# Kernel optimization log

Hardware: AMD Instinct MI355X
Metric: run time of the kernel (lower is better)

## Reference

```python
import jax, jax.numpy as jnp
import numpy as np

DIM = 384
WIN = 7
HEADS = 12
N = WIN * WIN
B_ = 4096
NW = 64


def _relative_position_index(ws: int) -> np.ndarray:
    coords = np.stack(np.meshgrid(np.arange(ws), np.arange(ws), indexing='ij'))  # (2, ws, ws)
    flat = coords.reshape(2, -1)  # (2, N)
    rel = flat[:, :, None] - flat[:, None, :]  # (2, N, N)
    rel = rel.transpose(1, 2, 0).copy()  # (N, N, 2)
    rel[:, :, 0] += ws - 1
    rel[:, :, 1] += ws - 1
    rel[:, :, 0] *= 2 * ws - 1
    return rel.sum(-1).astype(np.int32)  # (N, N)


def setup_inputs() -> dict:
    key = jax.random.key(0)
    ks = jax.random.split(key, 6)
    x = jax.random.normal(ks[0], (B_, N, DIM), dtype=jnp.float32)
    mask = jnp.zeros((NW, N, N), dtype=jnp.float32)
    bias_table = 0.02 * jax.random.normal(ks[1], ((2 * WIN - 1) ** 2, HEADS), dtype=jnp.float32)
    qkv_w = jax.random.normal(ks[2], (3 * DIM, DIM), dtype=jnp.float32) / np.sqrt(DIM)
    qkv_b = jnp.zeros((3 * DIM,), dtype=jnp.float32)
    proj_w = jax.random.normal(ks[3], (DIM, DIM), dtype=jnp.float32) / np.sqrt(DIM)
    proj_b = jnp.zeros((DIM,), dtype=jnp.float32)
    rel_index = jnp.asarray(_relative_position_index(WIN))  # (N, N) int32
    return {"x": x, "mask": mask, "bias_table": bias_table, "qkv_w": qkv_w,
            "qkv_b": qkv_b, "proj_w": proj_w, "proj_b": proj_b, "rel_index": rel_index}


def reference(x, mask, bias_table, qkv_w, qkv_b, proj_w, proj_b, rel_index):
    Bw, n, c = x.shape
    h = bias_table.shape[1]
    d = c // h
    scale = d ** (-0.5)
    # qkv projection: (Bw, n, 3, h, d)
    qkv = (x @ qkv_w.T + qkv_b).reshape(Bw, n, 3, h, d)
    qkv = jnp.transpose(qkv, (2, 0, 3, 1, 4))  # (3, Bw, h, n, d)
    q, k, v = qkv[0], qkv[1], qkv[2]
    attn = jnp.einsum('bhqd,bhkd->bhqk', q * scale, k)  # (Bw, h, n, n)
    bias = bias_table[rel_index]  # (n, n, h)
    attn = attn + jnp.transpose(bias, (2, 0, 1))[None]  # broadcast over Bw
    nW = mask.shape[0]
    attn = attn.reshape(Bw // nW, nW, h, n, n) + mask[None, :, None]
    attn = attn.reshape(Bw, h, n, n)
    attn = jax.nn.softmax(attn, axis=-1)
    out = jnp.einsum('bhqk,bhkd->bhqd', attn, v)  # (Bw, h, n, d)
    out = jnp.transpose(out, (0, 2, 1, 3)).reshape(Bw, n, c)
    return out @ proj_w.T + proj_b
```

## Files before the change

kernel.cpp:

```cpp
#include <hip/hip_runtime.h>
#include <hip/hip_bf16.h>

#define DIM   384
#define NWIN  49
#define HEADS 12
#define SCALE 0.17677669529663687f

typedef unsigned short ushort;
using bf16x8 = __attribute__((ext_vector_type(8))) short;
using u16x4  = __attribute__((ext_vector_type(4))) ushort;
using f32x4  = __attribute__((ext_vector_type(4))) float;

__device__ __forceinline__ ushort f2bf(float f) {
  unsigned u = __float_as_uint(f);
  u += 0x7fff + ((u >> 16) & 1);
  return (ushort)(u >> 16);
}

typedef __attribute__((address_space(1))) const void gas_void;
typedef __attribute__((address_space(3))) void las_void;

__device__ __forceinline__ void gload16(const ushort* g, ushort* l) {
  __builtin_amdgcn_global_load_lds((gas_void*)g, (las_void*)l, 16, 0, 0);
}

__global__ void prep_kernel(const float* __restrict__ qkv_w, const float* __restrict__ proj_w,
                            const float* __restrict__ bias_table, const int* __restrict__ rel_index,
                            const float* __restrict__ mask, const float* __restrict__ qkv_b,
                            ushort* __restrict__ wqb, ushort* __restrict__ wpb,
                            float* __restrict__ qbF, float* __restrict__ bmF) {
  int i0 = blockIdx.x * 256 + threadIdx.x;
  int stride = gridDim.x * 256;
  for (int i = i0; i < 1152 * 384; i += stride) {
    float v = qkv_w[i];
    if (i < 384 * 384) v *= SCALE;
    wqb[i] = f2bf(v);
  }
  for (int i = i0; i < 384 * 384; i += stride) wpb[i] = f2bf(proj_w[i]);
  for (int i = i0; i < 1152; i += stride) qbF[i] = qkv_b[i] * (i < 384 ? SCALE : 1.f);
  for (int i = i0; i < 64 * HEADS * 4 * 4 * 64 * 4; i += stride) {
    int r = i & 3, lane = (i >> 2) & 63, kt = (i >> 8) & 3, wq = (i >> 10) & 3;
    int hw = i >> 12;
    int h = hw % HEADS, wdx = hw / HEADS;
    int q = wq * 16 + (lane >> 4) * 4 + r;
    int key = kt * 16 + (lane & 15);
    float v;
    if (q < NWIN)
      v = (key < NWIN) ? bias_table[rel_index[q * NWIN + key] * HEADS + h]
                         + mask[wdx * (NWIN * NWIN) + q * NWIN + key]
                       : -3.0e38f;
    else
      v = 0.f;
    bmF[i] = v;
  }
}

__global__ __launch_bounds__(256, 2) void qkv_attn_kernel(
    const float* __restrict__ x, const float* __restrict__ qbF,
    const ushort* __restrict__ wqb, const float* __restrict__ bmF,
    ushort* __restrict__ aog)
{
  __shared__ ushort wb[2 * 12288];
  __shared__ ushort qs[64 * 36];
  __shared__ ushort ks[64 * 36];
  __shared__ ushort vt[32 * 74];

  const int blk = blockIdx.x;
  const int tid = threadIdx.x;
  const int w = tid >> 6, l = tid & 63;
  const int c = l & 15, g = l >> 4;
  const int wm = w >> 1, wn = w & 1;
  const int wq = w;
  const int wdx = blk & 63;
  const float LOG2E = 1.4426950408889634f;

  auto stage_qkv = [&](int h, int kc, int buf) {
    #pragma unroll
    for (int s = 0; s < 6; ++s) {
      int i = s * 256 + tid;
      int n = i >> 4, g16 = i & 15;
      int grow = (n >> 5) * 384 + h * 32 + (n & 31);
      int sg = (g16 & 8) | ((g16 & 7) ^ (n & 7));
      gload16(wqb + (size_t)grow * DIM + kc * 128 + (sg << 3),
              wb + buf * 12288 + i * 8);
    }
  };

  bf16x8 areg[2][12] = {};
  auto compute_qkv = [&](int kcC, int buf, f32x4 (&acc)[2][3]) {
    const ushort* wcb = wb + buf * 12288;
    #pragma unroll
    for (int kk = 0; kk < 4; ++kk) {
      int sB = ((kk * 4 + g) ^ (c & 7)) << 3;
      #pragma unroll
      for (int nt = 0; nt < 3; ++nt) {
        int n = (wn * 3 + nt) * 16 + c;
        bf16x8 bb = *(const bf16x8*)&wcb[n * 128 + sB];
        acc[0][nt] = __builtin_amdgcn_mfma_f32_16x16x32_bf16(areg[0][kcC * 4 + kk], bb, acc[0][nt], 0, 0, 0);
        acc[1][nt] = __builtin_amdgcn_mfma_f32_16x16x32_bf16(areg[1][kcC * 4 + kk], bb, acc[1][nt], 0, 0, 0);
      }
    }
  };

  {
    const float* xb = x + (size_t)blk * (NWIN * DIM);
    for (int i = tid; i < 4704; i += 256) {
      float4 f = ((const float4*)xb)[i];
      int row = i / 96, c4 = i - row * 96;
      u16x4 v4 = { f2bf(f.x), f2bf(f.y), f2bf(f.z), f2bf(f.w) };
      *(u16x4*)&wb[row * 384 + c4 * 4] = v4;
    }
  }
  __syncthreads();
  #pragma unroll
  for (int mt = 0; mt < 2; ++mt) {
    int row = wm * 32 + mt * 16 + c;
    if (row < NWIN) {
      #pragma unroll
      for (int kg = 0; kg < 12; ++kg)
        areg[mt][kg] = *(const bf16x8*)&wb[row * 384 + kg * 32 + g * 8];
    }
  }
  __syncthreads();
  stage_qkv(0, 0, 0);
  stage_qkv(0, 1, 1);
  __syncthreads();

  for (int h = 0; h < HEADS; ++h) {
    f32x4 acc[2][3] = {};
    const int par = h & 1;

    compute_qkv(0, par, acc);
    __syncthreads();
    stage_qkv(h, 2, par);

    compute_qkv(1, par ^ 1, acc);
    __syncthreads();
    if (h < 11) stage_qkv(h + 1, 0, par ^ 1);

    compute_qkv(2, par, acc);
    __syncthreads();
    if (h < 11) stage_qkv(h + 1, 1, par);

    #pragma unroll
    for (int nt = 0; nt < 3; ++nt) {
      int gnt = wn * 3 + nt;
      int which = gnt >> 1;
      int d = (gnt & 1) * 16 + c;
      float qb_ = qbF[which * 384 + h * 32 + d];
      #pragma unroll
      for (int mt = 0; mt < 2; ++mt) {
        #pragma unroll
        for (int r = 0; r < 4; ++r) {
          int tok = wm * 32 + mt * 16 + g * 4 + r;
          float v = acc[mt][nt][r] + qb_;
          if (which == 0)      qs[tok * 36 + d] = f2bf(v);
          else if (which == 1) ks[tok * 36 + d] = f2bf(v);
          else                 vt[d * 74 + tok] = f2bf(v);
        }
      }
    }
    __syncthreads();

    const f32x4* bw4 = (const f32x4*)(bmF + ((((size_t)(wdx * HEADS + h)) * 4 + wq) * 4 * 64 + l) * 4);
    f32x4 bmv[4];
    #pragma unroll
    for (int kt = 0; kt < 4; ++kt) bmv[kt] = bw4[kt * 64];

    f32x4 sacc[4] = {};
    {
      bf16x8 aq = *(const bf16x8*)&qs[(wq * 16 + c) * 36 + g * 8];
      #pragma unroll
      for (int kt = 0; kt < 4; ++kt) {
        bf16x8 bk = *(const bf16x8*)&ks[(kt * 16 + c) * 36 + g * 8];
        sacc[kt] = __builtin_amdgcn_mfma_f32_16x16x32_bf16(aq, bk, sacc[kt], 0, 0, 0);
      }
    }
    float p[4][4];
    #pragma unroll
    for (int r = 0; r < 4; ++r) {
      float s0 = sacc[0][r] + bmv[0][r], s1 = sacc[1][r] + bmv[1][r];
      float s2 = sacc[2][r] + bmv[2][r], s3 = sacc[3][r] + bmv[3][r];
      float mx = fmaxf(fmaxf(s0, s1), fmaxf(s2, s3));
      mx = fmaxf(mx, __shfl_xor(mx, 1, 64));
      mx = fmaxf(mx, __shfl_xor(mx, 2, 64));
      mx = fmaxf(mx, __shfl_xor(mx, 4, 64));
      mx = fmaxf(mx, __shfl_xor(mx, 8, 64));
      float p0 = __builtin_exp2f((s0 - mx) * LOG2E);
      float p1 = __builtin_exp2f((s1 - mx) * LOG2E);
      float p2 = __builtin_exp2f((s2 - mx) * LOG2E);
      float p3 = __builtin_exp2f((s3 - mx) * LOG2E);
      float sum = p0 + p1 + p2 + p3;
      sum += __shfl_xor(sum, 1, 64);
      sum += __shfl_xor(sum, 2, 64);
      sum += __shfl_xor(sum, 4, 64);
      sum += __shfl_xor(sum, 8, 64);
      float inv = 1.0f / sum;
      p[0][r] = p0 * inv; p[1][r] = p1 * inv; p[2][r] = p2 * inv; p[3][r] = p3 * inv;
    }
    f32x4 pacc[2] = {};
    #pragma unroll
    for (int kkh = 0; kkh < 2; ++kkh) {
      #pragma unroll
      for (int t = 0; t < 2; ++t) {
        int kt = kkh * 2 + t;
        #pragma unroll
        for (int r = 0; r < 4; ++r)
          qs[(wq * 16 + g * 4 + r) * 36 + t * 16 + c] = f2bf(p[kt][r]);
      }
      bf16x8 ap = *(const bf16x8*)&qs[(wq * 16 + c) * 36 + g * 8];
      #pragma unroll
      for (int dt = 0; dt < 2; ++dt) {
        bf16x8 bv = *(const bf16x8*)&vt[(dt * 16 + c) * 74 + kkh * 32 + g * 8];
        pacc[dt] = __builtin_amdgcn_mfma_f32_16x16x32_bf16(ap, bv, pacc[dt], 0, 0, 0);
      }
    }
    #pragma unroll
    for (int dt = 0; dt < 2; ++dt) {
      #pragma unroll
      for (int rr = 0; rr < 4; ++rr) {
        int tok = wq * 16 + g * 4 + rr;
        if (tok < NWIN)
          aog[((size_t)blk * NWIN + tok) * DIM + h * 32 + dt * 16 + c] = f2bf(pacc[dt][rr]);
      }
    }
    __syncthreads();
  }
}

__global__ __launch_bounds__(256, 2) void proj_kernel(
    const ushort* __restrict__ ao, const ushort* __restrict__ wpb,
    const float* __restrict__ proj_b, float* __restrict__ out)
{
  extern __shared__ ushort sm3[];
  ushort* lA = sm3;
  ushort* lB = sm3 + 16384;

  const int blk = blockIdx.x;
  const int bM = blk / 3, bN = blk - bM * 3;
  const int m0 = bM * 128, n0 = bN * 128;
  const int tid = threadIdx.x;
  const int w = tid >> 6, l = tid & 63;
  const int c = l & 15, g = l >> 4;
  const int wm = w >> 1, wn = w & 1;

  auto stageA = [&](int kc, int buf) {
    #pragma unroll
    for (int s = 0; s < 4; ++s) {
      int i = s * 256 + tid;
      int row = i >> 3, g16 = i & 7;
      gload16(ao + (size_t)(m0 + row) * DIM + kc * 64 + ((g16 ^ (row & 7)) << 3),
              lA + buf * 8192 + i * 8);
    }
  };
  auto stageB = [&](int kc, int buf) {
    #pragma unroll
    for (int s = 0; s < 4; ++s) {
      int i = s * 256 + tid;
      int row = i >> 3, g16 = i & 7;
      gload16(wpb + (size_t)(n0 + row) * DIM + kc * 64 + ((g16 ^ (row & 7)) << 3),
              lB + buf * 8192 + i * 8);
    }
  };

  f32x4 acc[4][4] = {};
  stageA(0, 0); stageB(0, 0);
  stageA(1, 1); stageB(1, 1);
  __syncthreads();

  for (int kc = 0; kc < 6; ++kc) {
    const ushort* A = lA + (kc & 1) * 8192;
    const ushort* B = lB + (kc & 1) * 8192;
    #pragma unroll
    for (int kk = 0; kk < 2; ++kk) {
      int swz = ((kk * 4 + g) ^ (c & 7)) << 3;
      bf16x8 af[4], bfr[4];
      #pragma unroll
      for (int mt = 0; mt < 4; ++mt)
        af[mt] = *(const bf16x8*)&A[(wm * 64 + mt * 16 + c) * 64 + swz];
      #pragma unroll
      for (int nt = 0; nt < 4; ++nt)
        bfr[nt] = *(const bf16x8*)&B[(wn * 64 + nt * 16 + c) * 64 + swz];
      #pragma unroll
      for (int mt = 0; mt < 4; ++mt)
        #pragma unroll
        for (int nt = 0; nt < 4; ++nt)
          acc[mt][nt] = __builtin_amdgcn_mfma_f32_16x16x32_bf16(af[mt], bfr[nt], acc[mt][nt], 0, 0, 0);
    }
    __syncthreads();
    if (kc + 2 < 6) { stageA(kc + 2, kc & 1); stageB(kc + 2, kc & 1); }
  }

  #pragma unroll
  for (int nt = 0; nt < 4; ++nt) {
    int col = n0 + wn * 64 + nt * 16 + c;
    float pb = proj_b[col];
    #pragma unroll
    for (int mt = 0; mt < 4; ++mt) {
      #pragma unroll
      for (int r = 0; r < 4; ++r) {
        int row = m0 + wm * 64 + mt * 16 + g * 4 + r;
        out[(size_t)row * DIM + col] = acc[mt][nt][r] + pb;
      }
    }
  }
}

#define WB_OFF 0
#define QS_OFF 24576
#define KS_OFF 29696
#define VT_OFF 34816
#define AO_OFF 39424
#define SMEM_US 77056

__global__ __launch_bounds__(512, 2) void winattn_fused(
    const float* __restrict__ x, const float* __restrict__ qbF,
    const float* __restrict__ proj_b, const ushort* __restrict__ wqb,
    const ushort* __restrict__ wpb, const float* __restrict__ bmF,
    float* __restrict__ out)
{
  extern __shared__ ushort smem[];
  ushort* wb = smem + WB_OFF;
  ushort* ao = smem + AO_OFF;

  const int blk = blockIdx.x;
  const int tid = threadIdx.x;
  const int w = tid >> 6, l = tid & 63;
  const int c = l & 15, g = l >> 4;
  const int wm = w >> 1, wn = w & 1;
  const int win = w >> 2, wq = w & 3;
  const float LOG2E = 1.4426950408889634f;

  ushort* qsw = smem + QS_OFF + win * 2560;
  ushort* ksw = smem + KS_OFF + win * 2560;
  ushort* vtw = smem + VT_OFF + win * 2304;
  ushort* psw = qsw;

  auto stage_qkv = [&](int h, int kc, int buf) {
    #pragma unroll
    for (int s = 0; s < 3; ++s) {
      int i = s * 512 + tid;
      int n = i >> 4, g16 = i & 15;
      int grow = (n >> 5) * 384 + h * 32 + (n & 31);
      int sg = (g16 & 8) | ((g16 & 7) ^ (n & 7));
      gload16(wqb + (size_t)grow * DIM + kc * 128 + (sg << 3), wb + buf * 12288 + i * 8);
    }
  };
  auto stage_proj = [&](int nb, int kc, int buf) {
    #pragma unroll
    for (int s = 0; s < 3; ++s) {
      int i = s * 512 + tid;
      int n = i >> 4, g16 = i & 15;
      int grow = nb * 96 + n;
      int sg = (g16 & 8) | ((g16 & 7) ^ (n & 7));
      gload16(wpb + (size_t)grow * DIM + kc * 128 + (sg << 3), wb + buf * 12288 + i * 8);
    }
  };

  bf16x8 areg[2][12] = {};
  auto compute_qkv = [&](int kcC, int buf, f32x4 (&acc)[2][3]) {
    const ushort* wcb = wb + buf * 12288;
    #pragma unroll
    for (int kk = 0; kk < 4; ++kk) {
      int sB = ((kk * 4 + g) ^ (c & 7)) << 3;
      #pragma unroll
      for (int nt = 0; nt < 3; ++nt) {
        int n = (wn * 3 + nt) * 16 + c;
        bf16x8 bb = *(const bf16x8*)&wcb[n * 128 + sB];
        acc[0][nt] = __builtin_amdgcn_mfma_f32_16x16x32_bf16(areg[0][kcC * 4 + kk], bb, acc[0][nt], 0, 0, 0);
        acc[1][nt] = __builtin_amdgcn_mfma_f32_16x16x32_bf16(areg[1][kcC * 4 + kk], bb, acc[1][nt], 0, 0, 0);
      }
    }
  };
  auto compute_proj = [&](int kcC, int buf, f32x4 (&acc)[2][3]) {
    const ushort* wcb = wb + buf * 12288;
    int r0 = wm * 32 + c;      if (r0 >= 98) r0 -= 64;
    int r1 = wm * 32 + 16 + c; if (r1 >= 98) r1 -= 64;
    #pragma unroll
    for (int kk = 0; kk < 4; ++kk) {
      int p = kcC * 16 + kk * 4 + g;
      int sw = (p ^ (c & 7)) << 3;
      bf16x8 a0 = *(const bf16x8*)&ao[r0 * 384 + sw];
      bf16x8 a1 = *(const bf16x8*)&ao[r1 * 384 + sw];
      int sB = ((kk * 4 + g) ^ (c & 7)) << 3;
      #pragma unroll
      for (int nt = 0; nt < 3; ++nt) {
        int n = (wn * 3 + nt) * 16 + c;
        bf16x8 bb = *(const bf16x8*)&wcb[n * 128 + sB];
        acc[0][nt] = __builtin_amdgcn_mfma_f32_16x16x32_bf16(a0, bb, acc[0][nt], 0, 0, 0);
        acc[1][nt] = __builtin_amdgcn_mfma_f32_16x16x32_bf16(a1, bb, acc[1][nt], 0, 0, 0);
      }
    }
  };

  stage_qkv(0, 0, 0);
  stage_qkv(0, 1, 1);
  {
    const float* xb = x + (size_t)blk * (2 * NWIN * DIM);
    for (int i = tid; i < 9408; i += 512) {
      float4 f = ((const float4*)xb)[i];
      int row = i / 96, c4 = i - row * 96;
      int k = c4 * 4;
      int gr = k >> 3;
      u16x4 v4 = { f2bf(f.x), f2bf(f.y), f2bf(f.z), f2bf(f.w) };
      *(u16x4*)&ao[row * 384 + ((gr ^ (row & 7)) << 3) + (k & 7)] = v4;
    }
  }
  __syncthreads();
  #pragma unroll
  for (int mt = 0; mt < 2; ++mt) {
    int row = wm * 32 + mt * 16 + c;
    int wi = row >> 6, tok = row & 63;
    if (tok < NWIN) {
      int ar = wi * 49 + tok;
      #pragma unroll
      for (int kg = 0; kg < 12; ++kg)
        areg[mt][kg] = *(const bf16x8*)&ao[ar * 384 + (((kg * 4 + g) ^ (ar & 7)) << 3)];
    }
  }

  for (int h = 0; h < HEADS; ++h) {
    f32x4 acc[2][3] = {};
    const int par = h & 1;
    compute_qkv(0, par, acc);
    __syncthreads();
    stage_qkv(h, 2, par);
    compute_qkv(1, par ^ 1, acc);
    __syncthreads();
    if (h < 11) stage_qkv(h + 1, 0, par ^ 1); else stage_proj(0, 0, par ^ 1);
    compute_qkv(2, par, acc);
    __syncthreads();
    if (h < 11) stage_qkv(h + 1, 1, par); else stage_proj(0, 1, par);
    {
      int winE = wm >> 1;
      ushort* qsE = smem + QS_OFF + winE * 2560;
      ushort* ksE = smem + KS_OFF + winE * 2560;
      ushort* vtE = smem + VT_OFF + winE * 2304;
      #pragma unroll
      for (int nt = 0; nt < 3; ++nt) {
        int gnt = wn * 3 + nt;
        int which = gnt >> 1;
        int d = (gnt & 1) * 16 + c;
        float qb_ = qbF[which * 384 + h * 32 + d];
        #pragma unroll
        for (int mt = 0; mt < 2; ++mt) {
          #pragma unroll
          for (int r = 0; r < 4; ++r) {
            int tok = (wm & 1) * 32 + mt * 16 + g * 4 + r;
            float v = acc[mt][nt][r] + qb_;
            if (which == 0)      qsE[tok * 40 + d] = f2bf(v);
            else if (which == 1) ksE[tok * 40 + d] = f2bf(v);
            else                 vtE[d * 72 + tok] = f2bf(v);
          }
        }
      }
    }
    __syncthreads();

    const int wdx = ((blk << 1) + win) & 63;
    const f32x4* bw4 = (const f32x4*)(bmF + ((((size_t)(wdx * HEADS + h)) * 4 + wq) * 4 * 64 + l) * 4);
    f32x4 bmv[4];
    #pragma unroll
    for (int kt = 0; kt < 4; ++kt) bmv[kt] = bw4[kt * 64];

    f32x4 sacc[4] = {};
    {
      bf16x8 aq = *(const bf16x8*)&qsw[(wq * 16 + c) * 40 + g * 8];
      #pragma unroll
      for (int kt = 0; kt < 4; ++kt) {
        bf16x8 bk = *(const bf16x8*)&ksw[(kt * 16 + c) * 40 + g * 8];
        sacc[kt] = __builtin_amdgcn_mfma_f32_16x16x32_bf16(aq, bk, sacc[kt], 0, 0, 0);
      }
    }
    float p[4][4];
    #pragma unroll
    for (int r = 0; r < 4; ++r) {
      float s0 = sacc[0][r] + bmv[0][r], s1 = sacc[1][r] + bmv[1][r];
      float s2 = sacc[2][r] + bmv[2][r], s3 = sacc[3][r] + bmv[3][r];
      float mx = fmaxf(fmaxf(s0, s1), fmaxf(s2, s3));
      mx = fmaxf(mx, __shfl_xor(mx, 1, 64));
      mx = fmaxf(mx, __shfl_xor(mx, 2, 64));
      mx = fmaxf(mx, __shfl_xor(mx, 4, 64));
      mx = fmaxf(mx, __shfl_xor(mx, 8, 64));
      float p0 = __builtin_exp2f((s0 - mx) * LOG2E);
      float p1 = __builtin_exp2f((s1 - mx) * LOG2E);
      float p2 = __builtin_exp2f((s2 - mx) * LOG2E);
      float p3 = __builtin_exp2f((s3 - mx) * LOG2E);
      float sum = p0 + p1 + p2 + p3;
      sum += __shfl_xor(sum, 1, 64);
      sum += __shfl_xor(sum, 2, 64);
      sum += __shfl_xor(sum, 4, 64);
      sum += __shfl_xor(sum, 8, 64);
      float inv = 1.0f / sum;
      p[0][r] = p0 * inv; p[1][r] = p1 * inv; p[2][r] = p2 * inv; p[3][r] = p3 * inv;
    }
    f32x4 pacc2[2] = {};
    #pragma unroll
    for (int kkh = 0; kkh < 2; ++kkh) {
      #pragma unroll
      for (int t = 0; t < 2; ++t) {
        int kt = kkh * 2 + t;
        #pragma unroll
        for (int r = 0; r < 4; ++r)
          psw[(wq * 16 + g * 4 + r) * 40 + t * 16 + c] = f2bf(p[kt][r]);
      }
      bf16x8 ap = *(const bf16x8*)&psw[(wq * 16 + c) * 40 + g * 8];
      #pragma unroll
      for (int dt = 0; dt < 2; ++dt) {
        bf16x8 bv = *(const bf16x8*)&vtw[(dt * 16 + c) * 72 + kkh * 32 + g * 8];
        pacc2[dt] = __builtin_amdgcn_mfma_f32_16x16x32_bf16(ap, bv, pacc2[dt], 0, 0, 0);
      }
    }
    #pragma unroll
    for (int dt = 0; dt < 2; ++dt) {
      int gr0 = h * 4 + dt * 2 + (c >> 3);
      #pragma unroll
      for (int rr = 0; rr < 4; ++rr) {
        int tok = wq * 16 + g * 4 + rr;
        int row0 = win * 49 + tok;
        if (tok < NWIN)
          ao[row0 * 384 + (((gr0 ^ (row0 & 7)) << 3) | (c & 7))] = f2bf(pacc2[dt][rr]);
      }
    }
    __syncthreads();
  }

  __syncthreads();
  for (int nb = 0; nb < 4; ++nb) {
    f32x4 acc[2][3] = {};
    const int pb0 = (nb * 3) & 1;
    compute_proj(0, pb0, acc);
    __syncthreads();
    stage_proj(nb, 2, pb0);
    compute_proj(1, pb0 ^ 1, acc);
    __syncthreads();
    if (nb < 3) stage_proj(nb + 1, 0, pb0 ^ 1);
    compute_proj(2, pb0, acc);
    __syncthreads();
    if (nb < 3) stage_proj(nb + 1, 1, pb0);
    #pragma unroll
    for (int nt = 0; nt < 3; ++nt) {
      int col = nb * 96 + (wn * 3 + nt) * 16 + c;
      float pb = proj_b[col];
      #pragma unroll
      for (int mt = 0; mt < 2; ++mt) {
        #pragma unroll
        for (int r = 0; r < 4; ++r) {
          int mrow = wm * 32 + mt * 16 + g * 4 + r;
          if (mrow < 98) {
            int wi = mrow >= NWIN;
            int tok = mrow - (wi ? NWIN : 0);
            out[((size_t)((blk << 1) + wi) * NWIN + tok) * DIM + col] = acc[mt][nt][r] + pb;
          }
        }
      }
    }
  }
}

extern "C" void kernel_launch(void* const* d_in, const int* in_sizes, int n_in,
                              void* d_out, int out_size, void* d_ws, size_t ws_size,
                              hipStream_t stream) {
  const float* x          = (const float*)d_in[0];
  const float* mask       = (const float*)d_in[1];
  const float* bias_table = (const float*)d_in[2];
  const float* qkv_w      = (const float*)d_in[3];
  const float* qkv_b      = (const float*)d_in[4];
  const float* proj_w     = (const float*)d_in[5];
  const float* proj_b     = (const float*)d_in[6];
  const int*   rel_index  = (const int*)d_in[7];
  float* out = (float*)d_out;

  ushort* wqb = (ushort*)d_ws;
  ushort* wpb = (ushort*)((char*)d_ws + 884736);
  float*  qbF = (float*)((char*)d_ws + 1179648);
  float*  bmF = (float*)((char*)d_ws + 1184256);
  ushort* aog = (ushort*)((char*)d_ws + 13767168);
  const size_t NEED = 13767168ull + 154140672ull;

  prep_kernel<<<1024, 256, 0, stream>>>(qkv_w, proj_w, bias_table, rel_index, mask, qkv_b,
                                        wqb, wpb, qbF, bmF);

  if (ws_size >= NEED) {
    qkv_attn_kernel<<<4096, 256, 0, stream>>>(x, qbF, wqb, bmF, aog);
    hipFuncSetAttribute((const void*)proj_kernel,
                        hipFuncAttributeMaxDynamicSharedMemorySize, 65536);
    proj_kernel<<<4704, 256, 65536, stream>>>(aog, wpb, proj_b, out);
  } else {
    hipFuncSetAttribute((const void*)winattn_fused,
                        hipFuncAttributeMaxDynamicSharedMemorySize, SMEM_US * 2);
    winattn_fused<<<2048, 512, SMEM_US * 2, stream>>>(x, qbF, proj_b, wqb, wpb, bmF, out);
  }
}
```

Before: 798.6 us.

## Process two windows per block in qkv_attn kernel to share staged weights

The QKV+attention kernel now handles two windows per 512-thread block instead of one window per 256-thread block. Each head's weight slices, loaded into LDS, are reused by both windows, and the weight staging and barriers are amortized across both. Per-window q/k/v buffers use new padded strides in dynamic shared memory. The cost is a larger LDS footprint per block and bigger barriers across 8 waves, which may reduce occupancy.

After: 937.6 us. +17.4%, slower.

```diff
diff --git a/kernel.cpp b/kernel.cpp
--- a/kernel.cpp
+++ b/kernel.cpp
@@ -55,29 +55,32 @@
   }
 }
 
-__global__ __launch_bounds__(256, 2) void qkv_attn_kernel(
+#define WB_OFF 0
+#define QS_OFF 24576
+#define KS_OFF 29440
+#define VT_OFF 34304
+#define SMEM2_US 39040
+
+__global__ __launch_bounds__(512, 2) void qkv_attn_kernel(
     const float* __restrict__ x, const float* __restrict__ qbF,
     const ushort* __restrict__ wqb, const float* __restrict__ bmF,
     ushort* __restrict__ aog)
 {
-  __shared__ ushort wb[2 * 12288];
-  __shared__ ushort qs[64 * 36];
-  __shared__ ushort ks[64 * 36];
-  __shared__ ushort vt[32 * 74];
+  extern __shared__ ushort smem[];
+  ushort* wb = smem + WB_OFF;
 
   const int blk = blockIdx.x;
   const int tid = threadIdx.x;
   const int w = tid >> 6, l = tid & 63;
   const int c = l & 15, g = l >> 4;
   const int wm = w >> 1, wn = w & 1;
-  const int wq = w;
-  const int wdx = blk & 63;
+  const int win = w >> 2, wq = w & 3;
   const float LOG2E = 1.4426950408889634f;
 
   auto stage_qkv = [&](int h, int kc, int buf) {
     #pragma unroll
-    for (int s = 0; s < 6; ++s) {
-      int i = s * 256 + tid;
+    for (int s = 0; s < 3; ++s) {
+      int i = s * 512 + tid;
       int n = i >> 4, g16 = i & 15;
       int grow = (n >> 5) * 384 + h * 32 + (n & 31);
       int sg = (g16 & 8) | ((g16 & 7) ^ (n & 7));
@@ -102,26 +105,28 @@
     }
   };
 
-  {
-    const float* xb = x + (size_t)blk * (NWIN * DIM);
-    for (int i = tid; i < 4704; i += 256) {
+  #pragma unroll
+  for (int wi = 0; wi < 2; ++wi) {
+    const float* xb = x + (size_t)((blk << 1) + wi) * (NWIN * DIM);
+    for (int i = tid; i < 4704; i += 512) {
       float4 f = ((const float4*)xb)[i];
       int row = i / 96, c4 = i - row * 96;
       u16x4 v4 = { f2bf(f.x), f2bf(f.y), f2bf(f.z), f2bf(f.w) };
       *(u16x4*)&wb[row * 384 + c4 * 4] = v4;
     }
-  }
-  __syncthreads();
-  #pragma unroll
-  for (int mt = 0; mt < 2; ++mt) {
-    int row = wm * 32 + mt * 16 + c;
-    if (row < NWIN) {
-      #pragma unroll
-      for (int kg = 0; kg < 12; ++kg)
-        areg[mt][kg] = *(const bf16x8*)&wb[row * 384 + kg * 32 + g * 8];
-    }
-  }
-  __syncthreads();
+    __syncthreads();
+    #pragma unroll
+    for (int mt = 0; mt < 2; ++mt) {
+      int row = wm * 32 + mt * 16 + c;
+      int tok = row & 63;
+      if ((row >> 6) == wi && tok < NWIN) {
+        #pragma unroll
+        for (int kg = 0; kg < 12; ++kg)
+          areg[mt][kg] = *(const bf16x8*)&wb[tok * 384 + kg * 32 + g * 8];
+      }
+    }
+    __syncthreads();
+  }
   stage_qkv(0, 0, 0);
   stage_qkv(0, 1, 1);
   __syncthreads();
@@ -142,26 +147,36 @@
     __syncthreads();
     if (h < 11) stage_qkv(h + 1, 1, par);
 
-    #pragma unroll
-    for (int nt = 0; nt < 3; ++nt) {
-      int gnt = wn * 3 + nt;
-      int which = gnt >> 1;
-      int d = (gnt & 1) * 16 + c;
-      float qb_ = qbF[which * 384 + h * 32 + d];
-      #pragma unroll
-      for (int mt = 0; mt < 2; ++mt) {
+    {
+      int winE = wm >> 1;
+      ushort* qsE = smem + QS_OFF + winE * 2432;
+      ushort* ksE = smem + KS_OFF + winE * 2432;
+      ushort* vtE = smem + VT_OFF + winE * 2368;
+      #pragma unroll
+      for (int nt = 0; nt < 3; ++nt) {
+        int gnt = wn * 3 + nt;
+        int which = gnt >> 1;
+        int d = (gnt & 1) * 16 + c;
+        float qb_ = qbF[which * 384 + h * 32 + d];
         #pragma unroll
-        for (int r = 0; r < 4; ++r) {
-          int tok = wm * 32 + mt * 16 + g * 4 + r;
-          float v = acc[mt][nt][r] + qb_;
-          if (which == 0)      qs[tok * 36 + d] = f2bf(v);
-          else if (which == 1) ks[tok * 36 + d] = f2bf(v);
-          else                 vt[d * 74 + tok] = f2bf(v);
+        for (int mt = 0; mt < 2; ++mt) {
+          #pragma unroll
+          for (int r = 0; r < 4; ++r) {
+            int tok = (wm & 1) * 32 + mt * 16 + g * 4 + r;
+            float v = acc[mt][nt][r] + qb_;
+            if (which == 0)      qsE[tok * 38 + d] = f2bf(v);
+            else if (which == 1) ksE[tok * 38 + d] = f2bf(v);
+            else                 vtE[d * 74 + tok] = f2bf(v);
+          }
         }
       }
     }
     __syncthreads();
 
+    ushort* qsw = smem + QS_OFF + win * 2432;
+    ushort* ksw = smem + KS_OFF + win * 2432;
+    ushort* vtw = smem + VT_OFF + win * 2368;
+    const int wdx = ((blk << 1) + win) & 63;
     const f32x4* bw4 = (const f32x4*)(bmF + ((((size_t)(wdx * HEADS + h)) * 4 + wq) * 4 * 64 + l) * 4);
     f32x4 bmv[4];
     #pragma unroll
@@ -169,10 +184,10 @@
 
     f32x4 sacc[4] = {};
     {
-      bf16x8 aq = *(const bf16x8*)&qs[(wq * 16 + c) * 36 + g * 8];
+      bf16x8 aq = *(const bf16x8*)&qsw[(wq * 16 + c) * 38 + g * 8];
       #pragma unroll
       for (int kt = 0; kt < 4; ++kt) {
-        bf16x8 bk = *(const bf16x8*)&ks[(kt * 16 + c) * 36 + g * 8];
+        bf16x8 bk = *(const bf16x8*)&ksw[(kt * 16 + c) * 38 + g * 8];
         sacc[kt] = __builtin_amdgcn_mfma_f32_16x16x32_bf16(aq, bk, sacc[kt], 0, 0, 0);
       }
     }
@@ -206,12 +221,12 @@
         int kt = kkh * 2 + t;
         #pragma unroll
         for (int r = 0; r < 4; ++r)
-          qs[(wq * 16 + g * 4 + r) * 36 + t * 16 + c] = f2bf(p[kt][r]);
-      }
-      bf16x8 ap = *(const bf16x8*)&qs[(wq * 16 + c) * 36 + g * 8];
+          qsw[(wq * 16 + g * 4 + r) * 38 + t * 16 + c] = f2bf(p[kt][r]);
+      }
+      bf16x8 ap = *(const bf16x8*)&qsw[(wq * 16 + c) * 38 + g * 8];
       #pragma unroll
       for (int dt = 0; dt < 2; ++dt) {
-        bf16x8 bv = *(const bf16x8*)&vt[(dt * 16 + c) * 74 + kkh * 32 + g * 8];
+        bf16x8 bv = *(const bf16x8*)&vtw[(dt * 16 + c) * 74 + kkh * 32 + g * 8];
         pacc[dt] = __builtin_amdgcn_mfma_f32_16x16x32_bf16(ap, bv, pacc[dt], 0, 0, 0);
       }
     }
@@ -221,7 +236,8 @@
       for (int rr = 0; rr < 4; ++rr) {
         int tok = wq * 16 + g * 4 + rr;
         if (tok < NWIN)
-          aog[((size_t)blk * NWIN + tok) * DIM + h * 32 + dt * 16 + c] = f2bf(pacc[dt][rr]);
+          aog[((size_t)((blk << 1) + win) * NWIN + tok) * DIM + h * 32 + dt * 16 + c] =
+              f2bf(pacc[dt][rr]);
       }
     }
     __syncthreads();
@@ -306,12 +322,12 @@
   }
 }
 
-#define WB_OFF 0
-#define QS_OFF 24576
-#define KS_OFF 29696
-#define VT_OFF 34816
-#define AO_OFF 39424
-#define SMEM_US 77056
+#define FWB_OFF 0
+#define FQS_OFF 24576
+#define FKS_OFF 29696
+#define FVT_OFF 34816
+#define FAO_OFF 39424
+#define FSMEM_US 77056
 
 __global__ __launch_bounds__(512, 2) void winattn_fused(
     const float* __restrict__ x, const float* __restrict__ qbF,
@@ -320,8 +336,8 @@
     float* __restrict__ out)
 {
   extern __shared__ ushort smem[];
-  ushort* wb = smem + WB_OFF;
-  ushort* ao = smem + AO_OFF;
+  ushort* wb = smem + FWB_OFF;
+  ushort* ao = smem + FAO_OFF;
 
   const int blk = blockIdx.x;
   const int tid = threadIdx.x;
@@ -331,9 +347,9 @@
   const int win = w >> 2, wq = w & 3;
   const float LOG2E = 1.4426950408889634f;
 
-  ushort* qsw = smem + QS_OFF + win * 2560;
-  ushort* ksw = smem + KS_OFF + win * 2560;
-  ushort* vtw = smem + VT_OFF + win * 2304;
+  ushort* qsw = smem + FQS_OFF + win * 2560;
+  ushort* ksw = smem + FKS_OFF + win * 2560;
+  ushort* vtw = smem + FVT_OFF + win * 2304;
   ushort* psw = qsw;
 
   auto stage_qkv = [&](int h, int kc, int buf) {
@@ -433,9 +449,9 @@
     if (h < 11) stage_qkv(h + 1, 1, par); else stage_proj(0, 1, par);
     {
       int winE = wm >> 1;
-      ushort* qsE = smem + QS_OFF + winE * 2560;
-      ushort* ksE = smem + KS_OFF + winE * 2560;
-      ushort* vtE = smem + VT_OFF + winE * 2304;
+      ushort* qsE = smem + FQS_OFF + winE * 2560;
+      ushort* ksE = smem + FKS_OFF + winE * 2560;
+      ushort* vtE = smem + FVT_OFF + winE * 2304;
       #pragma unroll
       for (int nt = 0; nt < 3; ++nt) {
         int gnt = wn * 3 + nt;
@@ -582,13 +598,15 @@
                                         wqb, wpb, qbF, bmF);
 
   if (ws_size >= NEED) {
-    qkv_attn_kernel<<<4096, 256, 0, stream>>>(x, qbF, wqb, bmF, aog);
+    hipFuncSetAttribute((const void*)qkv_attn_kernel,
+                        hipFuncAttributeMaxDynamicSharedMemorySize, SMEM2_US * 2);
+    qkv_attn_kernel<<<2048, 512, SMEM2_US * 2, stream>>>(x, qbF, wqb, bmF, aog);
     hipFuncSetAttribute((const void*)proj_kernel,
                         hipFuncAttributeMaxDynamicSharedMemorySize, 65536);
     proj_kernel<<<4704, 256, 65536, stream>>>(aog, wpb, proj_b, out);
   } else {
     hipFuncSetAttribute((const void*)winattn_fused,
-                        hipFuncAttributeMaxDynamicSharedMemorySize, SMEM_US * 2);
-    winattn_fused<<<2048, 512, SMEM_US * 2, stream>>>(x, qbF, proj_b, wqb, wpb, bmF, out);
+                        hipFuncAttributeMaxDynamicSharedMemorySize, FSMEM_US * 2);
+    winattn_fused<<<2048, 512, FSMEM_US * 2, stream>>>(x, qbF, proj_b, wqb, wpb, bmF, out);
   }
 }
```
